# Kernel optimization log

Measured on AMD Instinct MI355X. Metric: run time of the kernel, lower is better.

## Reference

```python
import jax, jax.numpy as jnp
import numpy as np

N_NODES = 100000
N_EDGES = 1600000
D = 128
BN_EPS = 1e-5
GINE_EPS = 0.0  # GINEConv default eps=0, train_eps=False


def setup_inputs() -> dict:
    key = jax.random.key(0)
    ks = jax.random.split(key, 9)
    x = jax.random.normal(ks[0], (N_NODES, D), dtype=jnp.float32)
    edge_index = jax.random.randint(ks[1], (2, N_EDGES), 0, N_NODES, dtype=jnp.int64)
    edge_attr = jax.random.normal(ks[2], (N_EDGES, D), dtype=jnp.float32)
    s = 1.0 / np.sqrt(D)
    W1 = jax.random.uniform(ks[3], (D, D), jnp.float32, -s, s)
    b1 = jax.random.uniform(ks[4], (D,), jnp.float32, -s, s)
    W2 = jax.random.uniform(ks[5], (D, D), jnp.float32, -s, s)
    b2 = jax.random.uniform(ks[6], (D,), jnp.float32, -s, s)
    gamma = jnp.ones((D,), jnp.float32)
    beta = jnp.zeros((D,), jnp.float32)
    return {"x": x, "edge_index": edge_index, "edge_attr": edge_attr,
            "W1": W1, "b1": b1, "W2": W2, "b2": b2,
            "gamma": gamma, "beta": beta}


def reference(x, edge_index, edge_attr, W1, b1, W2, b2, gamma, beta):
    src, dst = edge_index[0], edge_index[1]
    # per-edge message: ReLU(x_j + e_ij)
    msg = jax.nn.relu(x[src] + edge_attr)                      # [E, D]
    # sum aggregation to target nodes
    agg = jax.ops.segment_sum(msg, dst, num_segments=x.shape[0])  # [N, D]
    h = (1.0 + GINE_EPS) * x + agg
    # MLP: Linear -> ReLU -> Linear
    h = jax.nn.relu(h @ W1 + b1) @ W2 + b2
    # BatchNorm1d (training mode: batch stats, biased variance)
    mean = jnp.mean(h, axis=0)
    var = jnp.var(h, axis=0)
    h = (h - mean) * jax.lax.rsqrt(var + BN_EPS) * gamma + beta
    return jax.nn.relu(h)
```

## Files before the change

### kernel.cpp

```cpp
#include <hip/hip_runtime.h>

#define BN_EPS 1e-5f

typedef __bf16 bf16;
typedef __bf16 bf16x8 __attribute__((ext_vector_type(8)));
typedef __bf16 bf16x4 __attribute__((ext_vector_type(4)));
typedef float f32x4 __attribute__((ext_vector_type(4)));

__global__ void xprep_kernel(const float4* __restrict__ x4, bf16x4* __restrict__ xb4, int n4) {
    int i = blockIdx.x * blockDim.x + threadIdx.x;
    const int stride = gridDim.x * blockDim.x;
    for (; i < n4; i += stride) {
        const float4 v = x4[i];
        bf16x4 o;
        o[0] = (bf16)v.x; o[1] = (bf16)v.y; o[2] = (bf16)v.z; o[3] = (bf16)v.w;
        xb4[i] = o;
    }
}

__global__ void wprep_kernel(const float* __restrict__ W1, const float* __restrict__ W2,
                             bf16* __restrict__ Wt1, bf16* __restrict__ Wt2) {
    const int c = blockIdx.x;
    const int k = threadIdx.x;
    Wt1[c * 128 + k] = (bf16)W1[k * 128 + c];
    Wt2[c * 128 + k] = (bf16)W2[k * 128 + c];
}

__global__ void count_kernel(const int* __restrict__ ei, int* __restrict__ deg, int E) {
    int i = blockIdx.x * blockDim.x + threadIdx.x;
    const int stride = gridDim.x * blockDim.x;
    for (; i < E; i += stride) atomicAdd(&deg[ei[E + i]], 1);
}

__global__ void scanA(const int* __restrict__ deg, int* __restrict__ rowStart,
                      int* __restrict__ blockSums, int N) {
    __shared__ int sd[256];
    const int t = threadIdx.x;
    const int idx = blockIdx.x * 1024 + t * 4;
    int d0 = 0, d1 = 0, d2 = 0, d3 = 0;
    if (idx + 3 < N) { int4 v = *(const int4*)&deg[idx]; d0 = v.x; d1 = v.y; d2 = v.z; d3 = v.w; }
    else {
        if (idx     < N) d0 = deg[idx];
        if (idx + 1 < N) d1 = deg[idx + 1];
        if (idx + 2 < N) d2 = deg[idx + 2];
    }
    const int s = d0 + d1 + d2 + d3;
    sd[t] = s;
    __syncthreads();
    #pragma unroll
    for (int off = 1; off < 256; off <<= 1) {
        const int v = (t >= off) ? sd[t - off] : 0;
        __syncthreads();
        sd[t] += v;
        __syncthreads();
    }
    const int ex = sd[t] - s;
    if (idx     < N) rowStart[idx]     = ex;
    if (idx + 1 < N) rowStart[idx + 1] = ex + d0;
    if (idx + 2 < N) rowStart[idx + 2] = ex + d0 + d1;
    if (idx + 3 < N) rowStart[idx + 3] = ex + d0 + d1 + d2;
    if (t == 255) blockSums[blockIdx.x] = sd[255];
}

__global__ void scanB(int* __restrict__ blockSums, int nblk) {
    __shared__ int sd[256];
    const int t = threadIdx.x;
    const int s = (t < nblk) ? blockSums[t] : 0;
    sd[t] = s;
    __syncthreads();
    #pragma unroll
    for (int off = 1; off < 256; off <<= 1) {
        const int v = (t >= off) ? sd[t - off] : 0;
        __syncthreads();
        sd[t] += v;
        __syncthreads();
    }
    if (t < nblk) blockSums[t] = sd[t] - s;
}

__global__ void scanC(int* __restrict__ rowStart, int* __restrict__ cursor,
                      const int* __restrict__ blockSums, int N) {
    int i = blockIdx.x * blockDim.x + threadIdx.x;
    const int stride = gridDim.x * blockDim.x;
    for (; i < N; i += stride) {
        const int v = rowStart[i] + blockSums[i >> 10];
        rowStart[i] = v;
        cursor[i]   = v;
    }
}

__global__ void scatter_kernel(const int* __restrict__ ei, int* __restrict__ cursor,
                               int2* __restrict__ sPair, int E) {
    int i = blockIdx.x * blockDim.x + threadIdx.x;
    const int stride = gridDim.x * blockDim.x;
    for (; i < E; i += stride) {
        const int dst = ei[E + i];
        const int src = ei[i];
        const int pos = atomicAdd(&cursor[dst], 1);
        sPair[pos] = make_int2(i, src);
    }
}

__launch_bounds__(256)
__global__ void agg_kernel(const float* __restrict__ x, const bf16* __restrict__ xb,
                           const float* __restrict__ ea, const int2* __restrict__ sPair,
                           const int* __restrict__ rowStart, const int* __restrict__ deg,
                           bf16* __restrict__ h0b, int N) {
    const int wid = (blockIdx.x * blockDim.x + threadIdx.x) >> 6;
    if (wid >= N) return;
    const int lane = threadIdx.x & 63;
    const int half = lane >> 5;
    const int c    = lane & 31;

    const int rs = rowStart[wid];
    const int dg = deg[wid];

    f32x4 acc = {0.f, 0.f, 0.f, 0.f};

    int done = 0;
    while (done < dg) {
        const int batch = (dg - done < 64) ? (dg - done) : 64;
        int2 p = make_int2(0, 0);
        if (lane < batch) p = sPair[rs + done + lane];
        int i = 0;
        for (; i + 4 <= batch; i += 4) {
            const int eA = __shfl(p.x, i + half);
            const int sA = __shfl(p.y, i + half);
            const int eB = __shfl(p.x, i + 2 + half);
            const int sB = __shfl(p.y, i + 2 + half);
            const f32x4 a0 = __builtin_nontemporal_load((const f32x4*)ea + (((size_t)eA) << 5) + c);
            const bf16x4 x0 = *((const bf16x4*)xb + (((size_t)sA) << 5) + c);
            const f32x4 a1 = __builtin_nontemporal_load((const f32x4*)ea + (((size_t)eB) << 5) + c);
            const bf16x4 x1 = *((const bf16x4*)xb + (((size_t)sB) << 5) + c);
            acc[0] += fmaxf(a0[0] + (float)x0[0], 0.f) + fmaxf(a1[0] + (float)x1[0], 0.f);
            acc[1] += fmaxf(a0[1] + (float)x0[1], 0.f) + fmaxf(a1[1] + (float)x1[1], 0.f);
            acc[2] += fmaxf(a0[2] + (float)x0[2], 0.f) + fmaxf(a1[2] + (float)x1[2], 0.f);
            acc[3] += fmaxf(a0[3] + (float)x0[3], 0.f) + fmaxf(a1[3] + (float)x1[3], 0.f);
        }
        if (i + 2 <= batch) {
            const int eA = __shfl(p.x, i + half);
            const int sA = __shfl(p.y, i + half);
            const f32x4 a0 = __builtin_nontemporal_load((const f32x4*)ea + (((size_t)eA) << 5) + c);
            const bf16x4 x0 = *((const bf16x4*)xb + (((size_t)sA) << 5) + c);
            acc[0] += fmaxf(a0[0] + (float)x0[0], 0.f);
            acc[1] += fmaxf(a0[1] + (float)x0[1], 0.f);
            acc[2] += fmaxf(a0[2] + (float)x0[2], 0.f);
            acc[3] += fmaxf(a0[3] + (float)x0[3], 0.f);
            i += 2;
        }
        if (i < batch) {
            const int eA = __shfl(p.x, i);
            const int sA = __shfl(p.y, i);
            if (half == 0) {
                const f32x4 a0 = __builtin_nontemporal_load((const f32x4*)ea + (((size_t)eA) << 5) + c);
                const bf16x4 x0 = *((const bf16x4*)xb + (((size_t)sA) << 5) + c);
                acc[0] += fmaxf(a0[0] + (float)x0[0], 0.f);
                acc[1] += fmaxf(a0[1] + (float)x0[1], 0.f);
                acc[2] += fmaxf(a0[2] + (float)x0[2], 0.f);
                acc[3] += fmaxf(a0[3] + (float)x0[3], 0.f);
            }
        }
        done += batch;
    }

    acc[0] += __shfl_xor(acc[0], 32);
    acc[1] += __shfl_xor(acc[1], 32);
    acc[2] += __shfl_xor(acc[2], 32);
    acc[3] += __shfl_xor(acc[3], 32);

    if (half == 0) {
        const f32x4 xv = *((const f32x4*)x + (((size_t)wid) << 5) + c);
        bf16x4 o;
        o[0] = (bf16)(acc[0] + xv[0]);
        o[1] = (bf16)(acc[1] + xv[1]);
        o[2] = (bf16)(acc[2] + xv[2]);
        o[3] = (bf16)(acc[3] + xv[3]);
        *((bf16x4*)h0b + (((size_t)wid) << 5) + c) = o;
    }
}

__launch_bounds__(256, 1)
__global__ void mlp_kernel(const bf16* __restrict__ h0b,
                           const bf16* __restrict__ Wt1, const float* __restrict__ b1,
                           const bf16* __restrict__ Wt2, const float* __restrict__ b2,
                           float* __restrict__ out, double* __restrict__ stats, int N) {
    __shared__ bf16 Xs[128][136];
    __shared__ float SredS[4][128];
    __shared__ float SredQ[4][128];
    const int tid  = threadIdx.x;
    const int lane = tid & 63;
    const int wv   = tid >> 6;
    const int base = blockIdx.x * 128;

    {
        const int r  = tid >> 1;
        const int c0 = (tid & 1) * 64;
        const int n  = base + r;
        bf16x8* dst = (bf16x8*)&Xs[r][c0];
        if (n < N) {
            const bf16x8* src = (const bf16x8*)(h0b + (size_t)n * 128 + c0);
            #pragma unroll
            for (int q = 0; q < 8; q++) dst[q] = src[q];
        } else {
            bf16x8 z;
            #pragma unroll
            for (int k = 0; k < 8; k++) z[k] = (bf16)0.f;
            #pragma unroll
            for (int q = 0; q < 8; q++) dst[q] = z;
        }
    }

    const int colq = lane & 15;
    const int kq   = lane >> 4;
    f32x4 accm[2][8];
    #pragma unroll
    for (int tr = 0; tr < 2; tr++)
        #pragma unroll
        for (int tc = 0; tc < 8; tc++) accm[tr][tc] = (f32x4){0.f, 0.f, 0.f, 0.f};

    #pragma unroll
    for (int ks = 0; ks < 4; ks++) {
        const int ko = 32 * ks + kq * 8;
        const bf16x8 a0 = *(const bf16x8*)&Xs[32 * wv + colq][ko];
        const bf16x8 a1 = *(const bf16x8*)&Xs[32 * wv + 16 + colq][ko];
        #pragma unroll
        for (int tc = 0; tc < 8; tc++) {
            const bf16x8 bf = *(const bf16x8*)&Wt1[(size_t)(16 * tc + colq) * 128 + ko];
            accm[0][tc] = __builtin_amdgcn_mfma_f32_16x16x32_bf16(a0, bf, accm[0][tc], 0, 0, 0);
            accm[1][tc] = __builtin_amdgcn_mfma_f32_16x16x32_bf16(a1, bf, accm[1][tc], 0, 0, 0);
        }
    }

    #pragma unroll
    for (int tc = 0; tc < 8; tc++) {
        const float bj = b1[16 * tc + colq];
        #pragma unroll
        for (int tr = 0; tr < 2; tr++) {
            #pragma unroll
            for (int r = 0; r < 4; r++) {
                const int row = 32 * wv + 16 * tr + 4 * kq + r;
                Xs[row][16 * tc + colq] = (bf16)fmaxf(accm[tr][tc][r] + bj, 0.f);
            }
        }
    }

    #pragma unroll
    for (int tr = 0; tr < 2; tr++)
        #pragma unroll
        for (int tc = 0; tc < 8; tc++) accm[tr][tc] = (f32x4){0.f, 0.f, 0.f, 0.f};

    #pragma unroll
    for (int ks = 0; ks < 4; ks++) {
        const int ko = 32 * ks + kq * 8;
        const bf16x8 a0 = *(const bf16x8*)&Xs[32 * wv + colq][ko];
        const bf16x8 a1 = *(const bf16x8*)&Xs[32 * wv + 16 + colq][ko];
        #pragma unroll
        for (int tc = 0; tc < 8; tc++) {
            const bf16x8 bf = *(const bf16x8*)&Wt2[(size_t)(16 * tc + colq) * 128 + ko];
            accm[0][tc] = __builtin_amdgcn_mfma_f32_16x16x32_bf16(a0, bf, accm[0][tc], 0, 0, 0);
            accm[1][tc] = __builtin_amdgcn_mfma_f32_16x16x32_bf16(a1, bf, accm[1][tc], 0, 0, 0);
        }
    }

    #pragma unroll
    for (int tc = 0; tc < 8; tc++) {
        const int col = 16 * tc + colq;
        const float bj = b2[col];
        float sv = 0.f, qv = 0.f;
        #pragma unroll
        for (int tr = 0; tr < 2; tr++) {
            #pragma unroll
            for (int r = 0; r < 4; r++) {
                const int n = base + 32 * wv + 16 * tr + 4 * kq + r;
                if (n < N) {
                    const float h2 = accm[tr][tc][r] + bj;
                    out[(size_t)n * 128 + col] = h2;
                    sv += h2; qv += h2 * h2;
                }
            }
        }
        sv += __shfl_xor(sv, 16); qv += __shfl_xor(qv, 16);
        sv += __shfl_xor(sv, 32); qv += __shfl_xor(qv, 32);
        if (kq == 0) {
            SredS[wv][col] = sv;
            SredQ[wv][col] = qv;
        }
    }

    __syncthreads();
    if (tid < 128) {
        const float ss = SredS[0][tid] + SredS[1][tid] + SredS[2][tid] + SredS[3][tid];
        const float qq = SredQ[0][tid] + SredQ[1][tid] + SredQ[2][tid] + SredQ[3][tid];
        unsafeAtomicAdd(&stats[tid],       (double)ss);
        unsafeAtomicAdd(&stats[128 + tid], (double)qq);
    }
}

__global__ void bnprep_kernel(const double* __restrict__ stats, const float* __restrict__ gamma,
                              const float* __restrict__ beta, float* __restrict__ sb, float invN) {
    const int c = threadIdx.x;
    const float mean = (float)(stats[c] * (double)invN);
    const float ex2  = (float)(stats[128 + c] * (double)invN);
    const float var  = ex2 - mean * mean;
    const float rstd = rsqrtf(var + BN_EPS);
    const float sc = rstd * gamma[c];
    sb[c] = sc;
    sb[128 + c] = beta[c] - mean * sc;
}

__global__ void bn_kernel(float4* __restrict__ out4, const float* __restrict__ sb, int n4) {
    int i = blockIdx.x * blockDim.x + threadIdx.x;
    const int stride = gridDim.x * blockDim.x;
    for (; i < n4; i += stride) {
        const int c4 = (i & 31) << 2;
        float4 v = out4[i];
        const float4 sc = *(const float4*)&sb[c4];
        const float4 bs = *(const float4*)&sb[128 + c4];
        v.x = fmaxf(fmaf(v.x, sc.x, bs.x), 0.f);
        v.y = fmaxf(fmaf(v.y, sc.y, bs.y), 0.f);
        v.z = fmaxf(fmaf(v.z, sc.z, bs.z), 0.f);
        v.w = fmaxf(fmaf(v.w, sc.w, bs.w), 0.f);
        out4[i] = v;
    }
}

extern "C" void kernel_launch(void* const* d_in, const int* in_sizes, int n_in,
                              void* d_out, int out_size, void* d_ws, size_t ws_size,
                              hipStream_t stream) {
    const float* x     = (const float*)d_in[0];
    const int*   ei    = (const int*)d_in[1];
    const float* ea    = (const float*)d_in[2];
    const float* W1    = (const float*)d_in[3];
    const float* b1    = (const float*)d_in[4];
    const float* W2    = (const float*)d_in[5];
    const float* b2    = (const float*)d_in[6];
    const float* gamma = (const float*)d_in[7];
    const float* beta  = (const float*)d_in[8];
    float* out = (float*)d_out;

    const int N = in_sizes[0] / 128;
    const int E = in_sizes[1] / 2;

    char* w = (char*)d_ws;
    size_t o = 0;
    int* deg = (int*)(w + o);         o += ((size_t)N * 4 + 15) & ~(size_t)15;
    const size_t zeroLen = o + 2048;
    double* stats = (double*)(w + o); o += 2048;
    float*  sb    = (float*)(w + o);  o += 1024;
    int* rowStart = (int*)(w + o);    o += ((size_t)N * 4 + 15) & ~(size_t)15;
    int* cursor   = (int*)(w + o);    o += ((size_t)N * 4 + 15) & ~(size_t)15;
    int* blockSums= (int*)(w + o);    o += 1024;
    int2* sPair   = (int2*)(w + o);   o += (size_t)E * 8;
    bf16* Wt1     = (bf16*)(w + o);   o += 32768;
    bf16* Wt2     = (bf16*)(w + o);   o += 32768;
    bf16* xb      = (bf16*)(w + o);   o += (size_t)N * 128 * 2;
    bf16* h0b     = (bf16*)(w + o);   o += (size_t)N * 128 * 2;

    hipMemsetAsync(d_ws, 0, zeroLen, stream);

    xprep_kernel<<<2048, 256, 0, stream>>>((const float4*)x, (bf16x4*)xb, N * 32);
    wprep_kernel<<<128, 128, 0, stream>>>(W1, W2, Wt1, Wt2);

    const int nblk = (N + 1023) / 1024;
    count_kernel<<<2048, 256, 0, stream>>>(ei, deg, E);
    scanA<<<nblk, 256, 0, stream>>>(deg, rowStart, blockSums, N);
    scanB<<<1, 256, 0, stream>>>(blockSums, nblk);
    scanC<<<256, 256, 0, stream>>>(rowStart, cursor, blockSums, N);
    scatter_kernel<<<2048, 256, 0, stream>>>(ei, cursor, sPair, E);

    agg_kernel<<<(N * 64 + 255) / 256, 256, 0, stream>>>(x, xb, ea, sPair, rowStart, deg, h0b, N);

    mlp_kernel<<<(N + 127) / 128, 256, 0, stream>>>(h0b, Wt1, b1, Wt2, b2, out, stats, N);

    bnprep_kernel<<<1, 128, 0, stream>>>(stats, gamma, beta, sb, 1.0f / (float)N);

    bn_kernel<<<2048, 256, 0, stream>>>((float4*)out, sb, N * 32);
}
```

Before: 496.8 us.

## Merge prep kernels, fold BN prep into BN, deepen gather unroll, relax launch bounds

The degree-count and x-to-bf16 conversion kernels become one launch whose blocks split between the two jobs, and the single-block BN-statistics kernel is folded into the BN apply kernel, where each block recomputes scale and bias into shared memory. The edge-gather loop now issues eight edges' loads per iteration instead of four, putting more memory requests in flight. The mlp kernel's launch bounds drop the min-blocks hint, which may change register allocation. Together these cut launch overhead and raise memory-level parallelism, at the cost of redundant per-block BN prep and higher register pressure in the gather loop.

After: 498.6 us. Within noise of the previous version (+0.4%).

```diff
diff --git a/kernel.cpp b/kernel.cpp
--- a/kernel.cpp
+++ b/kernel.cpp
@@ -7,14 +7,20 @@
 typedef __bf16 bf16x4 __attribute__((ext_vector_type(4)));
 typedef float f32x4 __attribute__((ext_vector_type(4)));
 
-__global__ void xprep_kernel(const float4* __restrict__ x4, bf16x4* __restrict__ xb4, int n4) {
-    int i = blockIdx.x * blockDim.x + threadIdx.x;
-    const int stride = gridDim.x * blockDim.x;
-    for (; i < n4; i += stride) {
-        const float4 v = x4[i];
-        bf16x4 o;
-        o[0] = (bf16)v.x; o[1] = (bf16)v.y; o[2] = (bf16)v.z; o[3] = (bf16)v.w;
-        xb4[i] = o;
+__global__ void prep_kernel(const int* __restrict__ ei, int* __restrict__ deg, int E,
+                            const float4* __restrict__ x4, bf16x4* __restrict__ xb4, int n4) {
+    const int half = 2048 * 256;
+    if (blockIdx.x < 2048) {
+        int i = blockIdx.x * blockDim.x + threadIdx.x;
+        for (; i < E; i += half) atomicAdd(&deg[ei[E + i]], 1);
+    } else {
+        int i = (blockIdx.x - 2048) * blockDim.x + threadIdx.x;
+        for (; i < n4; i += half) {
+            const float4 v = x4[i];
+            bf16x4 o;
+            o[0] = (bf16)v.x; o[1] = (bf16)v.y; o[2] = (bf16)v.z; o[3] = (bf16)v.w;
+            xb4[i] = o;
+        }
     }
 }
 
@@ -24,12 +30,6 @@
     const int k = threadIdx.x;
     Wt1[c * 128 + k] = (bf16)W1[k * 128 + c];
     Wt2[c * 128 + k] = (bf16)W2[k * 128 + c];
-}
-
-__global__ void count_kernel(const int* __restrict__ ei, int* __restrict__ deg, int E) {
-    int i = blockIdx.x * blockDim.x + threadIdx.x;
-    const int stride = gridDim.x * blockDim.x;
-    for (; i < E; i += stride) atomicAdd(&deg[ei[E + i]], 1);
 }
 
 __global__ void scanA(const int* __restrict__ deg, int* __restrict__ rowStart,
@@ -123,7 +123,28 @@
         int2 p = make_int2(0, 0);
         if (lane < batch) p = sPair[rs + done + lane];
         int i = 0;
-        for (; i + 4 <= batch; i += 4) {
+        for (; i + 8 <= batch; i += 8) {
+            int e[4], s[4];
+            #pragma unroll
+            for (int q = 0; q < 4; q++) {
+                e[q] = __shfl(p.x, i + 2 * q + half);
+                s[q] = __shfl(p.y, i + 2 * q + half);
+            }
+            f32x4 a[4]; bf16x4 xr[4];
+            #pragma unroll
+            for (int q = 0; q < 4; q++) {
+                a[q]  = __builtin_nontemporal_load((const f32x4*)ea + (((size_t)e[q]) << 5) + c);
+                xr[q] = *((const bf16x4*)xb + (((size_t)s[q]) << 5) + c);
+            }
+            #pragma unroll
+            for (int q = 0; q < 4; q++) {
+                acc[0] += fmaxf(a[q][0] + (float)xr[q][0], 0.f);
+                acc[1] += fmaxf(a[q][1] + (float)xr[q][1], 0.f);
+                acc[2] += fmaxf(a[q][2] + (float)xr[q][2], 0.f);
+                acc[3] += fmaxf(a[q][3] + (float)xr[q][3], 0.f);
+            }
+        }
+        if (i + 4 <= batch) {
             const int eA = __shfl(p.x, i + half);
             const int sA = __shfl(p.y, i + half);
             const int eB = __shfl(p.x, i + 2 + half);
@@ -136,6 +157,7 @@
             acc[1] += fmaxf(a0[1] + (float)x0[1], 0.f) + fmaxf(a1[1] + (float)x1[1], 0.f);
             acc[2] += fmaxf(a0[2] + (float)x0[2], 0.f) + fmaxf(a1[2] + (float)x1[2], 0.f);
             acc[3] += fmaxf(a0[3] + (float)x0[3], 0.f) + fmaxf(a1[3] + (float)x1[3], 0.f);
+            i += 4;
         }
         if (i + 2 <= batch) {
             const int eA = __shfl(p.x, i + half);
@@ -179,7 +201,7 @@
     }
 }
 
-__launch_bounds__(256, 1)
+__launch_bounds__(256)
 __global__ void mlp_kernel(const bf16* __restrict__ h0b,
                            const bf16* __restrict__ Wt1, const float* __restrict__ b1,
                            const bf16* __restrict__ Wt2, const float* __restrict__ b2,
@@ -296,26 +318,29 @@
     }
 }
 
-__global__ void bnprep_kernel(const double* __restrict__ stats, const float* __restrict__ gamma,
-                              const float* __restrict__ beta, float* __restrict__ sb, float invN) {
-    const int c = threadIdx.x;
-    const float mean = (float)(stats[c] * (double)invN);
-    const float ex2  = (float)(stats[128 + c] * (double)invN);
-    const float var  = ex2 - mean * mean;
-    const float rstd = rsqrtf(var + BN_EPS);
-    const float sc = rstd * gamma[c];
-    sb[c] = sc;
-    sb[128 + c] = beta[c] - mean * sc;
-}
-
-__global__ void bn_kernel(float4* __restrict__ out4, const float* __restrict__ sb, int n4) {
-    int i = blockIdx.x * blockDim.x + threadIdx.x;
+__global__ void bn_kernel(float4* __restrict__ out4, const double* __restrict__ stats,
+                          const float* __restrict__ gamma, const float* __restrict__ beta,
+                          float invN, int n4) {
+    __shared__ float s_sc[128];
+    __shared__ float s_bs[128];
+    const int tid = threadIdx.x;
+    if (tid < 128) {
+        const float mean = (float)(stats[tid] * (double)invN);
+        const float ex2  = (float)(stats[128 + tid] * (double)invN);
+        const float var  = ex2 - mean * mean;
+        const float rstd = rsqrtf(var + BN_EPS);
+        const float sc = rstd * gamma[tid];
+        s_sc[tid] = sc;
+        s_bs[tid] = beta[tid] - mean * sc;
+    }
+    __syncthreads();
+    int i = blockIdx.x * blockDim.x + tid;
     const int stride = gridDim.x * blockDim.x;
     for (; i < n4; i += stride) {
         const int c4 = (i & 31) << 2;
         float4 v = out4[i];
-        const float4 sc = *(const float4*)&sb[c4];
-        const float4 bs = *(const float4*)&sb[128 + c4];
+        const float4 sc = *(const float4*)&s_sc[c4];
+        const float4 bs = *(const float4*)&s_bs[c4];
         v.x = fmaxf(fmaf(v.x, sc.x, bs.x), 0.f);
         v.y = fmaxf(fmaf(v.y, sc.y, bs.y), 0.f);
         v.z = fmaxf(fmaf(v.z, sc.z, bs.z), 0.f);
@@ -346,7 +371,6 @@
     int* deg = (int*)(w + o);         o += ((size_t)N * 4 + 15) & ~(size_t)15;
     const size_t zeroLen = o + 2048;
     double* stats = (double*)(w + o); o += 2048;
-    float*  sb    = (float*)(w + o);  o += 1024;
     int* rowStart = (int*)(w + o);    o += ((size_t)N * 4 + 15) & ~(size_t)15;
     int* cursor   = (int*)(w + o);    o += ((size_t)N * 4 + 15) & ~(size_t)15;
     int* blockSums= (int*)(w + o);    o += 1024;
@@ -358,11 +382,10 @@
 
     hipMemsetAsync(d_ws, 0, zeroLen, stream);
 
-    xprep_kernel<<<2048, 256, 0, stream>>>((const float4*)x, (bf16x4*)xb, N * 32);
+    prep_kernel<<<4096, 256, 0, stream>>>(ei, deg, E, (const float4*)x, (bf16x4*)xb, N * 32);
     wprep_kernel<<<128, 128, 0, stream>>>(W1, W2, Wt1, Wt2);
 
     const int nblk = (N + 1023) / 1024;
-    count_kernel<<<2048, 256, 0, stream>>>(ei, deg, E);
     scanA<<<nblk, 256, 0, stream>>>(deg, rowStart, blockSums, N);
     scanB<<<1, 256, 0, stream>>>(blockSums, nblk);
     scanC<<<256, 256, 0, stream>>>(rowStart, cursor, blockSums, N);
@@ -372,7 +395,5 @@
 
     mlp_kernel<<<(N + 127) / 128, 256, 0, stream>>>(h0b, Wt1, b1, Wt2, b2, out, stats, N);
 
-    bnprep_kernel<<<1, 128, 0, stream>>>(stats, gamma, beta, sb, 1.0f / (float)N);
-
-    bn_kernel<<<2048, 256, 0, stream>>>((float4*)out, sb, N * 32);
-}
+    bn_kernel<<<2048, 256, 0, stream>>>((float4*)out, stats, gamma, beta, 1.0f / (float)N, N * 32);
+}
```
